# Kernel optimization log

Measured on AMD Instinct MI355X. Metric: run time of the kernel, lower is better.

The kernel has to match this reference:

```python
import jax, jax.numpy as jnp
import numpy as np

NUM_EXPERTS = 8
IN_FEATURES = 1024
OUT_FEATURES = 1024
TOTAL_TOKENS = 8192


def setup_inputs() -> dict:
    key = jax.random.key(0)
    k_x, k_w, k_b = jax.random.split(key, 3)
    inputs = jax.random.normal(k_x, (TOTAL_TOKENS, IN_FEATURES), dtype=jnp.float32)
    # lecun_normal-style scale for the per-expert kernels
    kernel = jax.random.normal(k_w, (NUM_EXPERTS, IN_FEATURES, OUT_FEATURES), dtype=jnp.float32) / np.sqrt(IN_FEATURES)
    bias = jax.random.normal(k_b, (NUM_EXPERTS, OUT_FEATURES), dtype=jnp.float32) * 0.01
    # ragged group sizes that sum exactly to TOTAL_TOKENS (tokens pre-sorted by expert)
    rng = np.random.default_rng(0)
    gs = rng.multinomial(TOTAL_TOKENS, [1.0 / NUM_EXPERTS] * NUM_EXPERTS)
    group_sizes = jnp.asarray(gs, dtype=jnp.int32)
    return {"inputs": inputs, "group_sizes": group_sizes, "kernel": kernel, "bias": bias}


def reference(inputs, group_sizes, kernel, bias):
    # inputs: [T, in], kernel: [E, in, out], bias: [E, out], group_sizes: [E]
    E = kernel.shape[0]
    T = inputs.shape[0]
    # per-token expert id (tokens are sorted/grouped by expert)
    expert_ids = jnp.repeat(jnp.arange(E, dtype=jnp.int32), group_sizes, total_repeat_length=T)  # [T]
    onehot = jax.nn.one_hot(expert_ids, E, dtype=inputs.dtype)  # [T, E]
    # grouped ragged matmul: y[t] = x[t] @ W[expert_ids[t]]
    xe = jnp.einsum("te,ti->eti", onehot, inputs)  # [E, T, in], zero outside each expert's group
    y = jnp.einsum("eti,eio->to", xe, kernel)  # [T, out]
    # ragged bias expansion: bias of the owning expert per token
    y = y + jnp.take(bias, expert_ids, axis=0)
    return y
```

## Files before the change

### kernel.cpp

```cpp
#include <hip/hip_runtime.h>
#include <hip/hip_bf16.h>

#define KDIM 1024
#define NDIM 1024
#define NEXP 8
#define TTOK 8192
#define NT (KDIM / 32)

typedef __bf16 bf16x8 __attribute__((ext_vector_type(8)));
typedef __bf16 bf16x4 __attribute__((ext_vector_type(4)));
typedef float  f32x4  __attribute__((ext_vector_type(4)));

__device__ __forceinline__ void gl2lds16(const void* g, void* l) {
  __builtin_amdgcn_global_load_lds(
      (const __attribute__((address_space(1))) void*)g,
      (__attribute__((address_space(3))) void*)l, 16, 0, 0);
}


__global__ __launch_bounds__(256) void prepass_w(
    const float* __restrict__ W, __bf16* __restrict__ swB)
{
  __shared__ __align__(16) __bf16 Lt[64 * 72];
  const int t = threadIdx.x;
  int bid = blockIdx.x;
  int e = bid >> 8, r = bid & 255;
  int k0 = (r >> 4) * 64, n0 = (r & 15) * 64;
  const float* Wp = W + (size_t)e * KDIM * NDIM;
  int rr0 = t >> 4, c4 = t & 15;
#pragma unroll
  for (int p = 0; p < 4; ++p) {
    int kk = rr0 + p * 16;
    float4 v = *(const float4*)(Wp + (size_t)(k0 + kk) * NDIM + n0 + c4 * 4);
    Lt[(c4 * 4 + 0) * 72 + kk] = (__bf16)v.x;
    Lt[(c4 * 4 + 1) * 72 + kk] = (__bf16)v.y;
    Lt[(c4 * 4 + 2) * 72 + kk] = (__bf16)v.z;
    Lt[(c4 * 4 + 3) * 72 + kk] = (__bf16)v.w;
  }
  __syncthreads();
#pragma unroll
  for (int q = 0; q < 2; ++q) {
    int slot = q * 256 + t;
    int lane = slot & 63, grp = slot >> 6;
    int np = grp & 3, kt2 = grp >> 2;
    int nl = np * 16 + (lane & 15);
    int kl = kt2 * 32 + ((lane >> 4) << 3);
    bf16x8 v = *(const bf16x8*)(Lt + nl * 72 + kl);
    int panel = (n0 >> 4) + np;
    int ktg = (k0 >> 5) + kt2;
    size_t sg = (((size_t)e * 64 + panel) * 32 + ktg) * 64 + lane;
    *(bf16x8*)(swB + sg * 8) = v;
  }
}

__global__ __launch_bounds__(256, 3) void moe_gemm_lds(
    const float* __restrict__ x, const __bf16* __restrict__ swB,
    const int* __restrict__ gs, const float* __restrict__ bias,
    float* __restrict__ out)
{
  __shared__ __align__(16) __bf16 buf[3][8192];

  int y = blockIdx.y;
  int e = 0, tile0 = 0, lo = 0, hi = 0, found = 0, off = 0;
#pragma unroll
  for (int i = 0; i < NEXP; ++i) {
    int g = gs[i];
    int first = off >> 7;
    int cnt = (g > 0) ? (((off + g - 1) >> 7) - first + 1) : 0;
    if (!found) {
      if (y < cnt) {
        found = 1; e = i; tile0 = (first + y) << 7;
        lo = max(tile0, off); hi = min(tile0 + 128, off + g);
      } else y -= cnt;
    }
    off += g;
  }
  if (!found) return;
  const int n0 = blockIdx.x * 128;

  const int t = threadIdx.x, lane = t & 63, wv = t >> 6;
  const int wm = wv & 1, wn = wv >> 1, lm = lane & 15, lg = lane >> 4;

  const __bf16* gB0 = swB + (size_t)(e * 64 + (n0 >> 4) + wv) * 16384 + lane * 8;
  const __bf16* gB1 = swB + (size_t)(e * 64 + (n0 >> 4) + 4 + wv) * 16384 + lane * 8;

  auto stage_B = [&](int kt, int sb) {
    __bf16* l = &buf[sb][0];
    const int ko = kt * 512;
    gl2lds16(gB0 + ko, l + (size_t)(512 + wv * 64) * 8);
    gl2lds16(gB1 + ko, l + (size_t)(768 + wv * 64) * 8);
  };

  const float* xbase = x + (size_t)(tile0 + (t >> 3)) * KDIM + (t & 7) * 4;
  const int abase = (((t >> 7) * 64 + ((t & 7) >> 1) * 16 + ((t >> 3) & 15)) << 3) + (t & 1) * 4;

  auto issue_x = [&](int kt, float4* R) {
#pragma unroll
    for (int i = 0; i < 4; ++i)
      R[i] = *(const float4*)(xbase + (size_t)i * 32 * KDIM + kt * 32);
  };
  auto write_A = [&](int sb, const float4* R) {
    __bf16* l = &buf[sb][0] + abase;
#pragma unroll
    for (int i = 0; i < 4; ++i) {
      bf16x4 b;
      b[0] = (__bf16)R[i].x; b[1] = (__bf16)R[i].y;
      b[2] = (__bf16)R[i].z; b[3] = (__bf16)R[i].w;
      *(bf16x4*)(l + i * 1024) = b;
    }
  };

  f32x4 acc[4][4] = {};
  auto compute = [&](const __bf16* l) {
    bf16x8 aF[4], bF[4];
#pragma unroll
    for (int i = 0; i < 4; ++i)
      aF[i] = *(const bf16x8*)(l + (size_t)((wm * 4 + i) * 64 + lane) * 8);
#pragma unroll
    for (int j = 0; j < 4; ++j)
      bF[j] = *(const bf16x8*)(l + 4096 + (size_t)((wn * 4 + j) * 64 + lane) * 8);
#pragma unroll
    for (int i = 0; i < 4; ++i)
#pragma unroll
      for (int j = 0; j < 4; ++j)
        acc[i][j] = __builtin_amdgcn_mfma_f32_16x16x32_bf16(aF[i], bF[j], acc[i][j], 0, 0, 0);
  };

  {
    float4 R0[4];
    issue_x(0, R0);
    stage_B(0, 0);
    stage_B(1, 1);
    asm volatile("s_waitcnt vmcnt(4)" ::: "memory");
    write_A(0, R0);
  }

#pragma unroll 1
  for (int kt = 0; kt < NT; ++kt) {
    asm volatile("s_waitcnt vmcnt(2)" ::: "memory");
    asm volatile("s_waitcnt lgkmcnt(0)" ::: "memory");
    asm volatile("s_barrier" ::: "memory");

    float4 R[4];
    const bool havex = (kt + 1 < NT);
    if (havex) issue_x(kt + 1, R);
    if (kt + 2 < NT) stage_B(kt + 2, (kt + 2) % 3);
    __builtin_amdgcn_sched_barrier(0);

    __builtin_amdgcn_s_setprio(1);
    compute(&buf[kt % 3][0]);
    __builtin_amdgcn_s_setprio(0);

    if (havex) {
      if (kt + 2 < NT) asm volatile("s_waitcnt vmcnt(2)" ::: "memory");
      else             asm volatile("s_waitcnt vmcnt(0)" ::: "memory");
      write_A((kt + 1) % 3, R);
    }
  }

  float bj[4];
#pragma unroll
  for (int j = 0; j < 4; ++j) bj[j] = bias[e * NDIM + n0 + wn * 64 + j * 16 + lm];
#pragma unroll
  for (int i = 0; i < 4; ++i)
#pragma unroll
    for (int r = 0; r < 4; ++r) {
      int rabs = tile0 + wm * 64 + i * 16 + lg * 4 + r;
      if (rabs >= lo && rabs < hi) {
#pragma unroll
        for (int j = 0; j < 4; ++j)
          out[(size_t)rabs * NDIM + n0 + wn * 64 + j * 16 + lm] = acc[i][j][r] + bj[j];
      }
    }
}

#define LDA 40
__global__ __launch_bounds__(256) void moe_gemm_kernel(
    const float* __restrict__ x, const int* __restrict__ gs,
    const float* __restrict__ W, const float* __restrict__ bias,
    float* __restrict__ out)
{
  __shared__ __bf16 Al[128 * LDA];
  __shared__ __bf16 Bl[128 * LDA];
  const int e = blockIdx.z, mt = blockIdx.y, nt = blockIdx.x;
  int off = 0;
#pragma unroll
  for (int i = 0; i < NEXP; ++i) { int g = gs[i]; if (i < e) off += g; }
  const int ge = gs[e];
  const int m0 = mt * 128;
  if (m0 >= ge) return;
  const int rows = min(128, ge - m0);
  const int row0 = off + m0;
  const int n0 = nt * 128;
  const int t = threadIdx.x, lane = t & 63, wv = t >> 6;
  const int wm = wv & 1, wn = wv >> 1, lm = lane & 15, lg = lane >> 4;
  const int am = t >> 3, kq = t & 7, nb = t & 127, kh = t >> 7;
  float4 aReg[4]; float bReg[16];
  const float* Wp = W + (size_t)e * KDIM * NDIM + n0 + nb;
  auto load_tile = [&](int kt) {
#pragma unroll
    for (int p = 0; p < 4; ++p) {
      int r = am + 32 * p;
      if (r < rows) aReg[p] = *(const float4*)(x + (size_t)(row0 + r) * KDIM + kt * 32 + kq * 4);
      else aReg[p] = make_float4(0.f, 0.f, 0.f, 0.f);
    }
    const float* wp = Wp + (size_t)(kt * 32 + kh * 16) * NDIM;
#pragma unroll
    for (int j = 0; j < 16; ++j) bReg[j] = wp[(size_t)j * NDIM];
  };
  auto store_tile = [&]() {
#pragma unroll
    for (int p = 0; p < 4; ++p) {
      bf16x4 v;
      v[0] = (__bf16)aReg[p].x; v[1] = (__bf16)aReg[p].y;
      v[2] = (__bf16)aReg[p].z; v[3] = (__bf16)aReg[p].w;
      *(bf16x4*)(Al + (am + 32 * p) * LDA + kq * 4) = v;
    }
    bf16x8 b0, b1;
#pragma unroll
    for (int j = 0; j < 8; ++j) { b0[j] = (__bf16)bReg[j]; b1[j] = (__bf16)bReg[8 + j]; }
    *(bf16x8*)(Bl + nb * LDA + kh * 16) = b0;
    *(bf16x8*)(Bl + nb * LDA + kh * 16 + 8) = b1;
  };
  f32x4 acc[4][4] = {};
  load_tile(0);
#pragma unroll 1
  for (int kt = 0; kt < KDIM / 32; ++kt) {
    __syncthreads();
    store_tile();
    __syncthreads();
    if (kt + 1 < KDIM / 32) load_tile(kt + 1);
    bf16x8 af[4], bfr[4];
#pragma unroll
    for (int i = 0; i < 4; ++i)
      af[i] = *(const bf16x8*)(Al + (wm * 64 + i * 16 + lm) * LDA + lg * 8);
#pragma unroll
    for (int j = 0; j < 4; ++j)
      bfr[j] = *(const bf16x8*)(Bl + (wn * 64 + j * 16 + lm) * LDA + lg * 8);
#pragma unroll
    for (int i = 0; i < 4; ++i)
#pragma unroll
      for (int j = 0; j < 4; ++j)
        acc[i][j] = __builtin_amdgcn_mfma_f32_16x16x32_bf16(af[i], bfr[j], acc[i][j], 0, 0, 0);
  }
  float bj[4];
#pragma unroll
  for (int j = 0; j < 4; ++j) bj[j] = bias[e * NDIM + n0 + wn * 64 + j * 16 + lm];
#pragma unroll
  for (int i = 0; i < 4; ++i)
#pragma unroll
    for (int r = 0; r < 4; ++r) {
      int rr = wm * 64 + i * 16 + lg * 4 + r;
      if (rr < rows) {
#pragma unroll
        for (int j = 0; j < 4; ++j)
          out[(size_t)(row0 + rr) * NDIM + n0 + wn * 64 + j * 16 + lm] = acc[i][j][r] + bj[j];
      }
    }
}

extern "C" void kernel_launch(void* const* d_in, const int* in_sizes, int n_in,
                              void* d_out, int out_size, void* d_ws, size_t ws_size,
                              hipStream_t stream) {
  const float* x    = (const float*)d_in[0];
  const int*   gs   = (const int*)d_in[1];
  const float* W    = (const float*)d_in[2];
  const float* bias = (const float*)d_in[3];
  float*       out  = (float*)d_out;

  const size_t swB_bytes = (size_t)NEXP * KDIM * NDIM * 2;
  if (ws_size >= swB_bytes) {
    __bf16* swB = (__bf16*)d_ws;
    prepass_w<<<dim3(2048), 256, 0, stream>>>(W, swB);
    moe_gemm_lds<<<dim3(NDIM / 128, 72), 256, 0, stream>>>(x, swB, gs, bias, out);
  } else {
    moe_gemm_kernel<<<dim3(NDIM / 128, TTOK / 128, NEXP), 256, 0, stream>>>(x, gs, W, bias, out);
  }
}
```

Measured before the change: 148.3 us.

## Load A fragments directly into registers and remap blocks per XCD

Activation rows are now loaded from global memory straight into MFMA fragment registers and converted to bf16 in-register, so they no longer pass through LDS. Only the B tiles stay in the triple-buffered LDS ring, which halves shared memory use and removes the LDS writes and reads for A. The grid becomes 1D with an XCD-aware mapping that places the 9 row tiles of a column strip on the same XCD, to improve L2 reuse of weights. The cost is that each wave fetches its own A rows, so x is read once per wave column (twice per block), and the wait counts were restructured.

Result: slower. 199.6 us (+34.6%).

```diff
diff --git a/kernel.cpp b/kernel.cpp
--- a/kernel.cpp
+++ b/kernel.cpp
@@ -58,9 +58,13 @@
     const int* __restrict__ gs, const float* __restrict__ bias,
     float* __restrict__ out)
 {
-  __shared__ __align__(16) __bf16 buf[3][8192];
-
-  int y = blockIdx.y;
+  __shared__ __align__(16) __bf16 buf[3][4096];
+
+  const int b = blockIdx.x;
+  const int xcd = b & 7, bi = b >> 3;
+  int y = xcd * 9 + bi % 9;
+  const int nt = bi / 9;
+
   int e = 0, tile0 = 0, lo = 0, hi = 0, found = 0, off = 0;
 #pragma unroll
   for (int i = 0; i < NEXP; ++i) {
@@ -76,7 +80,7 @@
     off += g;
   }
   if (!found) return;
-  const int n0 = blockIdx.x * 128;
+  const int n0 = nt * 128;
 
   const int t = threadIdx.x, lane = t & 63, wv = t >> 6;
   const int wm = wv & 1, wn = wv >> 1, lm = lane & 15, lg = lane >> 4;
@@ -87,38 +91,39 @@
   auto stage_B = [&](int kt, int sb) {
     __bf16* l = &buf[sb][0];
     const int ko = kt * 512;
-    gl2lds16(gB0 + ko, l + (size_t)(512 + wv * 64) * 8);
-    gl2lds16(gB1 + ko, l + (size_t)(768 + wv * 64) * 8);
-  };
-
-  const float* xbase = x + (size_t)(tile0 + (t >> 3)) * KDIM + (t & 7) * 4;
-  const int abase = (((t >> 7) * 64 + ((t & 7) >> 1) * 16 + ((t >> 3) & 15)) << 3) + (t & 1) * 4;
-
-  auto issue_x = [&](int kt, float4* R) {
-#pragma unroll
-    for (int i = 0; i < 4; ++i)
-      R[i] = *(const float4*)(xbase + (size_t)i * 32 * KDIM + kt * 32);
-  };
-  auto write_A = [&](int sb, const float4* R) {
-    __bf16* l = &buf[sb][0] + abase;
+    gl2lds16(gB0 + ko, l + (size_t)(wv * 64) * 8);
+    gl2lds16(gB1 + ko, l + (size_t)((4 + wv) * 64) * 8);
+  };
+
+  const float* xA = x + (size_t)(tile0 + wm * 64 + lm) * KDIM + lg * 8;
+  float4 R[4][2];
+  auto issue_x = [&](int kt) {
 #pragma unroll
     for (int i = 0; i < 4; ++i) {
-      bf16x4 b;
-      b[0] = (__bf16)R[i].x; b[1] = (__bf16)R[i].y;
-      b[2] = (__bf16)R[i].z; b[3] = (__bf16)R[i].w;
-      *(bf16x4*)(l + i * 1024) = b;
+      const float* p = xA + (size_t)(i * 16) * KDIM + kt * 32;
+      R[i][0] = *(const float4*)p;
+      R[i][1] = *(const float4*)(p + 4);
+    }
+  };
+  bf16x8 aF[4];
+  auto convert_x = [&]() {
+#pragma unroll
+    for (int i = 0; i < 4; ++i) {
+      bf16x8 v;
+      v[0] = (__bf16)R[i][0].x; v[1] = (__bf16)R[i][0].y;
+      v[2] = (__bf16)R[i][0].z; v[3] = (__bf16)R[i][0].w;
+      v[4] = (__bf16)R[i][1].x; v[5] = (__bf16)R[i][1].y;
+      v[6] = (__bf16)R[i][1].z; v[7] = (__bf16)R[i][1].w;
+      aF[i] = v;
     }
   };
 
   f32x4 acc[4][4] = {};
   auto compute = [&](const __bf16* l) {
-    bf16x8 aF[4], bF[4];
-#pragma unroll
-    for (int i = 0; i < 4; ++i)
-      aF[i] = *(const bf16x8*)(l + (size_t)((wm * 4 + i) * 64 + lane) * 8);
+    bf16x8 bF[4];
 #pragma unroll
     for (int j = 0; j < 4; ++j)
-      bF[j] = *(const bf16x8*)(l + 4096 + (size_t)((wn * 4 + j) * 64 + lane) * 8);
+      bF[j] = *(const bf16x8*)(l + (size_t)((wn * 4 + j) * 64 + lane) * 8);
 #pragma unroll
     for (int i = 0; i < 4; ++i)
 #pragma unroll
@@ -126,37 +131,28 @@
         acc[i][j] = __builtin_amdgcn_mfma_f32_16x16x32_bf16(aF[i], bF[j], acc[i][j], 0, 0, 0);
   };
 
-  {
-    float4 R0[4];
-    issue_x(0, R0);
-    stage_B(0, 0);
-    stage_B(1, 1);
-    asm volatile("s_waitcnt vmcnt(4)" ::: "memory");
-    write_A(0, R0);
-  }
+  issue_x(0);
+  stage_B(0, 0);
+  asm volatile("s_waitcnt vmcnt(2)" ::: "memory");
+  convert_x();
+  issue_x(1);
+  stage_B(1, 1);
 
 #pragma unroll 1
-  for (int kt = 0; kt < NT; ++kt) {
+  for (int kt = 0; kt < NT - 1; ++kt) {
+    asm volatile("s_waitcnt vmcnt(10)" ::: "memory");
+    asm volatile("s_barrier" ::: "memory");
+    compute(&buf[kt % 3][0]);
     asm volatile("s_waitcnt vmcnt(2)" ::: "memory");
-    asm volatile("s_waitcnt lgkmcnt(0)" ::: "memory");
-    asm volatile("s_barrier" ::: "memory");
-
-    float4 R[4];
-    const bool havex = (kt + 1 < NT);
-    if (havex) issue_x(kt + 1, R);
-    if (kt + 2 < NT) stage_B(kt + 2, (kt + 2) % 3);
-    __builtin_amdgcn_sched_barrier(0);
-
-    __builtin_amdgcn_s_setprio(1);
-    compute(&buf[kt % 3][0]);
-    __builtin_amdgcn_s_setprio(0);
-
-    if (havex) {
-      if (kt + 2 < NT) asm volatile("s_waitcnt vmcnt(2)" ::: "memory");
-      else             asm volatile("s_waitcnt vmcnt(0)" ::: "memory");
-      write_A((kt + 1) % 3, R);
-    }
-  }
+    convert_x();
+    if (kt + 2 < NT) {
+      issue_x(kt + 2);
+      stage_B(kt + 2, (kt + 2) % 3);
+    }
+  }
+  asm volatile("s_waitcnt vmcnt(0)" ::: "memory");
+  asm volatile("s_barrier" ::: "memory");
+  compute(&buf[(NT - 1) % 3][0]);
 
   float bj[4];
 #pragma unroll
@@ -272,7 +268,7 @@
   if (ws_size >= swB_bytes) {
     __bf16* swB = (__bf16*)d_ws;
     prepass_w<<<dim3(2048), 256, 0, stream>>>(W, swB);
-    moe_gemm_lds<<<dim3(NDIM / 128, 72), 256, 0, stream>>>(x, swB, gs, bias, out);
+    moe_gemm_lds<<<dim3(576), 256, 0, stream>>>(x, swB, gs, bias, out);
   } else {
     moe_gemm_kernel<<<dim3(NDIM / 128, TTOK / 128, NEXP), 256, 0, stream>>>(x, gs, W, bias, out);
   }
```
